# Optimization experiments

Measured on AMD Instinct MI355X. Metric: run time of the kernel, lower is better.

## Reference

```python
import jax, jax.numpy as jnp
import numpy as np

B, C, H, W = 32, 64, 96, 96
RED = 8


def setup_inputs() -> dict:
    key = jax.random.key(0)
    k0, k1, k2 = jax.random.split(key, 3)
    x = jax.random.normal(k0, (B, C, H, W), dtype=jnp.float32)
    # 1x1 conv weights (squeezed to linear): conv1 C->C//RED, conv2 C//RED->C
    w1 = jax.random.normal(k1, (C // RED, C), dtype=jnp.float32) * (1.0 / np.sqrt(C))
    b1 = jnp.zeros((C // RED,), dtype=jnp.float32)
    w2 = jax.random.normal(k2, (C, C // RED), dtype=jnp.float32) * (1.0 / np.sqrt(C // RED))
    b2 = jnp.zeros((C,), dtype=jnp.float32)
    return {"x": x, "w1": w1, "b1": b1, "w2": w2, "b2": b2}


def reference(x, w1, b1, w2, b2):
    Bx, Cx, Hx, Wx = x.shape
    M = Hx * Wx
    # --- covariance pooling: x @ I_hat @ x^T == centered outer product / M ---
    xr = x.reshape(Bx, Cx, M)
    xc = xr - xr.mean(axis=-1, keepdims=True)
    cov = jnp.einsum('bcm,bdm->bcd', xc, xc) / M  # (B, C, C)
    # --- Newton-Schulz matrix sqrt, iteration = 5 ---
    I3 = 3.0 * jnp.eye(Cx, dtype=x.dtype)  # broadcast over batch
    normA = jnp.trace(cov, axis1=1, axis2=2)  # (1/3 * cov * 3I).sum == trace
    A = cov / normA[:, None, None]
    ZY = 0.5 * (I3 - A)
    Y = A @ ZY
    Z = ZY
    for _ in range(3):  # range(1, iteration-1) with iteration=5
        ZY = (0.5 * (I3 - Z)) @ Y
        Y = Y @ ZY
        Z = ZY @ Z
    ZY = 0.5 * (Y @ (I3 - Z @ Y))
    cov_sqrt = ZY * jnp.sqrt(normA)[:, None, None]  # (B, C, C)
    # --- channel gating ---
    s = cov_sqrt.mean(axis=1)  # mean over dim=1 -> (B, C)
    h = jax.nn.relu(s @ w1.T + b1)
    gate = jax.nn.sigmoid(h @ w2.T + b2)  # (B, C)
    return x * gate[:, :, None, None]
```

## Files before the change

### kernel.cpp

```cpp
#include <hip/hip_runtime.h>
#include <math.h>


#define BB 32
#define CC 64
#define MM 9216
#define NCHUNKS 16

typedef __attribute__((ext_vector_type(8))) short bf16x8;
typedef __attribute__((ext_vector_type(4))) float f32x4;

__device__ __forceinline__ short f2bf(float f) {
  unsigned u = __builtin_bit_cast(unsigned, f);
  return (short)(unsigned short)((u + 0x8000u) >> 16);
}
__device__ __forceinline__ float bf2f(short h) {
  unsigned u = ((unsigned)(unsigned short)h) << 16;
  return __builtin_bit_cast(float, u);
}
__device__ __forceinline__ void wt_store(float* p, float v) {
  __hip_atomic_store(p, v, __ATOMIC_RELAXED, __HIP_MEMORY_SCOPE_AGENT);
}

template <int NSTEP>
__device__ __forceinline__ void gram_body(const float* __restrict__ xb, int mwave,
                                          int quad, int col,
                                          f32x4 acc[4][4], float csum[4]) {
  const float* base[4];
#pragma unroll
  for (int rb = 0; rb < 4; rb++)
    base[rb] = xb + (size_t)(rb * 16 + col) * MM + mwave + quad * 8;

  float4 cur[4][2];
#pragma unroll
  for (int rb = 0; rb < 4; rb++) {
    cur[rb][0] = *(const float4*)(base[rb]);
    cur[rb][1] = *(const float4*)(base[rb] + 4);
  }
#pragma unroll
  for (int s = 0; s < NSTEP; s++) {
    float4 nxt[4][2];
    if (s + 1 < NSTEP) {
#pragma unroll
      for (int rb = 0; rb < 4; rb++) {
        const float* p = base[rb] + (s + 1) * 32;
        nxt[rb][0] = *(const float4*)(p);
        nxt[rb][1] = *(const float4*)(p + 4);
      }
    }
    bf16x8 frag[4];
#pragma unroll
    for (int rb = 0; rb < 4; rb++) {
      float v0 = cur[rb][0].x, v1 = cur[rb][0].y, v2 = cur[rb][0].z, v3 = cur[rb][0].w;
      float v4 = cur[rb][1].x, v5 = cur[rb][1].y, v6 = cur[rb][1].z, v7 = cur[rb][1].w;
      csum[rb] += ((v0 + v1) + (v2 + v3)) + ((v4 + v5) + (v6 + v7));
      bf16x8 f;
      f[0] = f2bf(v0); f[1] = f2bf(v1); f[2] = f2bf(v2); f[3] = f2bf(v3);
      f[4] = f2bf(v4); f[5] = f2bf(v5); f[6] = f2bf(v6); f[7] = f2bf(v7);
      frag[rb] = f;
    }
#pragma unroll
    for (int i = 0; i < 4; i++)
#pragma unroll
      for (int j = 0; j < 4; j++)
        acc[i][j] = __builtin_amdgcn_mfma_f32_16x16x32_bf16(frag[i], frag[j],
                                                            acc[i][j], 0, 0, 0);
    if (s + 1 < NSTEP) {
#pragma unroll
      for (int rb = 0; rb < 4; rb++) {
        cur[rb][0] = nxt[rb][0];
        cur[rb][1] = nxt[rb][1];
      }
    }
  }
}

__device__ __forceinline__ void mm64(short* __restrict__ D, const short* __restrict__ A,
                                     const short* __restrict__ Bm, int tid) {
  int w = tid >> 6, lane = tid & 63, quad = lane >> 4, col = lane & 15;
  f32x4 acc[4];
#pragma unroll
  for (int j = 0; j < 4; j++) acc[j] = (f32x4){0.f, 0.f, 0.f, 0.f};
#pragma unroll
  for (int ks = 0; ks < 2; ks++) {
    int k0 = ks * 32 + quad * 8;
    bf16x8 fa = *(const bf16x8*)(A + (w * 16 + col) * 64 + k0);
#pragma unroll
    for (int j = 0; j < 4; j++) {
      bf16x8 fb = *(const bf16x8*)(Bm + (j * 16 + col) * 64 + k0);
      acc[j] = __builtin_amdgcn_mfma_f32_16x16x32_bf16(fa, fb, acc[j], 0, 0, 0);
    }
  }
#pragma unroll
  for (int j = 0; j < 4; j++)
#pragma unroll
    for (int r = 0; r < 4; r++)
      D[(w * 16 + quad * 4 + r) * 64 + j * 16 + col] = f2bf(acc[j][r]);
}

__device__ __forceinline__ void mmcolsum(const short* __restrict__ A,
                                         const short* __restrict__ Bm,
                                         float* scol, int tid) {
  int w = tid >> 6, lane = tid & 63, quad = lane >> 4, col = lane & 15;
  f32x4 acc[4];
#pragma unroll
  for (int j = 0; j < 4; j++) acc[j] = (f32x4){0.f, 0.f, 0.f, 0.f};
#pragma unroll
  for (int ks = 0; ks < 2; ks++) {
    int k0 = ks * 32 + quad * 8;
    bf16x8 fa = *(const bf16x8*)(A + (w * 16 + col) * 64 + k0);
#pragma unroll
    for (int j = 0; j < 4; j++) {
      bf16x8 fb = *(const bf16x8*)(Bm + (j * 16 + col) * 64 + k0);
      acc[j] = __builtin_amdgcn_mfma_f32_16x16x32_bf16(fa, fb, acc[j], 0, 0, 0);
    }
  }
#pragma unroll
  for (int j = 0; j < 4; j++) {
    float t = (acc[j][0] + acc[j][1]) + (acc[j][2] + acc[j][3]);
    atomicAdd(&scol[j * 16 + col], t);
  }
}

__device__ __forceinline__ void ns_tail(unsigned char* smem, int b, int tid,
                                        const float* __restrict__ pg,
                                        const float* __restrict__ ps,
                                        const float* __restrict__ w1,
                                        const float* __restrict__ pb1,
                                        const float* __restrict__ w2,
                                        const float* __restrict__ pb2,
                                        float* __restrict__ gatews) {
  short* nb0 = (short*)smem;
  short* nb1 = nb0 + 4096;
  short* nb2 = nb0 + 8192;
  short* nb3 = nb0 + 12288;
  short* nb4 = nb0 + 16384;
  float* gsum = (float*)(smem + 40960);
  float* mu = (float*)(smem + 57344);
  float* scol = (float*)(smem + 57600);
  float* hbuf = (float*)(smem + 57856);
  float* pnorm = (float*)(smem + 57888);

  {
    const float4* pgb4 = (const float4*)(pg + (size_t)b * NCHUNKS * 4096);
    float4* gsum4 = (float4*)gsum;
#pragma unroll
    for (int e = 0; e < 4; e++) {
      int i4 = tid + 256 * e;
      float4 s = {0.f, 0.f, 0.f, 0.f};
#pragma unroll
      for (int c = 0; c < NCHUNKS; c++) {
        float4 v = pgb4[c * 1024 + i4];
        s.x += v.x; s.y += v.y; s.z += v.z; s.w += v.w;
      }
      gsum4[i4] = s;
    }
    if (tid < 64) {
      const float* psb = ps + (size_t)b * NCHUNKS * 256;
      float s = 0.f;
#pragma unroll
      for (int c = 0; c < NCHUNKS; c++)
#pragma unroll
        for (int sub = 0; sub < 4; sub++) s += psb[c * 256 + sub * 64 + tid];
      mu[tid] = s * (1.0f / MM);
    }
  }
  __syncthreads();

  if (tid < 64) {
    float d = gsum[tid * 65] * (1.0f / MM) - mu[tid] * mu[tid];
#pragma unroll
    for (int off = 32; off >= 1; off >>= 1) d += __shfl_down(d, off);
    if (tid == 0) *pnorm = d;
  }
  __syncthreads();
  float normA = *pnorm;
  float rn = 1.0f / normA;
#pragma unroll
  for (int e = 0; e < 16; e++) {
    int idx = tid + 256 * e;
    int r = idx >> 6, c = idx & 63;
    float cv = gsum[idx] * (1.0f / MM) - mu[r] * mu[c];
    float a = cv * rn;
    nb0[idx] = f2bf(a);
    nb1[idx] = f2bf((r == c ? 1.5f : 0.0f) - 0.5f * a);
  }
  __syncthreads();
  mm64(nb2, nb0, nb1, tid);
  __syncthreads();
  short *pY = nb2, *pZ = nb1, *s0 = nb3, *s1 = nb4, *s2 = nb0;
  for (int it = 0; it < 3; ++it) {
#pragma unroll
    for (int e = 0; e < 16; e++) {
      int idx = tid + 256 * e;
      int r = idx >> 6, c = idx & 63;
      float z = bf2f(pZ[idx]);
      s0[idx] = f2bf((r == c ? 1.5f : 0.0f) - 0.5f * z);
    }
    __syncthreads();
    mm64(s1, s0, pY, tid);
    __syncthreads();
    mm64(s2, pY, s1, tid);
    mm64(s0, s1, pZ, tid);
    __syncthreads();
    short* oY = pY; short* oZ = pZ; short* oW = s1;
    pY = s2; pZ = s0; s0 = oY; s1 = oZ; s2 = oW;
  }
  mm64(s0, pZ, pY, tid);
  __syncthreads();
#pragma unroll
  for (int e = 0; e < 16; e++) {
    int idx = tid + 256 * e;
    int r = idx >> 6, c = idx & 63;
    float p = bf2f(s0[idx]);
    s0[idx] = f2bf((r == c ? 3.0f : 0.0f) - p);
  }
  if (tid < 64) scol[tid] = 0.0f;
  __syncthreads();
  mmcolsum(pY, s0, scol, tid);
  __syncthreads();
  if (tid < 8) {
    float sc = 0.5f * sqrtf(normA) * (1.0f / 64.0f);
    float acc2 = pb1[tid];
    for (int c = 0; c < 64; c++) acc2 += scol[c] * sc * w1[tid * 64 + c];
    hbuf[tid] = fmaxf(acc2, 0.0f);
  }
  __syncthreads();
  if (tid < 64) {
    float acc2 = pb2[tid];
#pragma unroll
    for (int j = 0; j < 8; j++) acc2 += hbuf[j] * w2[tid * 8 + j];
    gatews[b * 64 + tid] = 1.0f / (1.0f + __expf(-acc2));
  }
}

__global__ __launch_bounds__(256, 2) void gramns_k(
    const float* __restrict__ x, float* __restrict__ pg, float* __restrict__ ps,
    int* __restrict__ ctr, const float* __restrict__ w1,
    const float* __restrict__ pb1, const float* __restrict__ w2,
    const float* __restrict__ pb2, float* __restrict__ gatews) {
  __shared__ __align__(16) unsigned char smem[65536];
  float(*red)[4096] = reinterpret_cast<float(*)[4096]>(smem);

  int b = blockIdx.x / NCHUNKS;
  int chunk = blockIdx.x % NCHUNKS;
  int tid = threadIdx.x;
  int w = tid >> 6, lane = tid & 63;
  int quad = lane >> 4, col = lane & 15;
  const float* xb = x + (size_t)b * CC * MM;

  f32x4 acc[4][4];
#pragma unroll
  for (int i = 0; i < 4; i++)
#pragma unroll
    for (int j = 0; j < 4; j++) acc[i][j] = (f32x4){0.f, 0.f, 0.f, 0.f};
  float csum[4] = {0.f, 0.f, 0.f, 0.f};

  if (chunk < 8) {
    int mwave = chunk * 640 + w * (5 * 32);
    gram_body<5>(xb, mwave, quad, col, acc, csum);
  } else {
    int mwave = 5120 + (chunk - 8) * 512 + w * (4 * 32);
    gram_body<4>(xb, mwave, quad, col, acc, csum);
  }

#pragma unroll
  for (int rb = 0; rb < 4; rb++) {
    float c0 = csum[rb];
    c0 += __shfl_xor(c0, 16);
    c0 += __shfl_xor(c0, 32);
    if (lane < 16)
      wt_store(ps + (size_t)blockIdx.x * 256 + w * 64 + rb * 16 + lane, c0);
  }

#pragma unroll
  for (int i = 0; i < 4; i++)
#pragma unroll
    for (int j = 0; j < 4; j++)
#pragma unroll
      for (int r = 0; r < 4; r++)
        red[w][(i * 16 + quad * 4 + r) * 64 + j * 16 + col] = acc[i][j][r];
  __syncthreads();
  float* covb = pg + (size_t)blockIdx.x * 4096;
#pragma unroll
  for (int e = 0; e < 16; e++) {
    int idx = tid + 256 * e;
    float v = (red[0][idx] + red[1][idx]) + (red[2][idx] + red[3][idx]);
    wt_store(covb + idx, v);
  }

  __syncthreads();
  volatile int* pold = (int*)smem;
  if (tid == 0)
    *pold = __hip_atomic_fetch_add(ctr + b, 1, __ATOMIC_RELAXED,
                                   __HIP_MEMORY_SCOPE_AGENT);
  __syncthreads();
  if (*pold != NCHUNKS - 1) return;

  __builtin_amdgcn_fence(__ATOMIC_ACQUIRE, "agent");
  ns_tail(smem, b, tid, pg, ps, w1, pb1, w2, pb2, gatews);
}

__global__ __launch_bounds__(256) void gate_mul(const float* __restrict__ x,
                                                const float* __restrict__ gatews,
                                                float* __restrict__ out) {
  int bc = blockIdx.x;
  float g = gatews[bc];
  const float4* xp = (const float4*)(x + (size_t)bc * MM);
  float4* op = (float4*)(out + (size_t)bc * MM);
  int t = threadIdx.x;
#pragma unroll
  for (int it = 0; it < 9; ++it) {
    float4 v = xp[t + it * 256];
    v.x *= g; v.y *= g; v.z *= g; v.w *= g;
    op[t + it * 256] = v;
  }
}

__global__ __launch_bounds__(256, 2) void gram_k_leg(const float* __restrict__ x,
                                                     float* __restrict__ pg,
                                                     float* __restrict__ ps) {
  int b = blockIdx.x / NCHUNKS;
  int chunk = blockIdx.x % NCHUNKS;
  int tid = threadIdx.x;
  int w = tid >> 6, lane = tid & 63;
  int quad = lane >> 4, col = lane & 15;
  const float* xb = x + (size_t)b * CC * MM;

  f32x4 acc[4][4];
#pragma unroll
  for (int i = 0; i < 4; i++)
#pragma unroll
    for (int j = 0; j < 4; j++) acc[i][j] = (f32x4){0.f, 0.f, 0.f, 0.f};
  float csum[4] = {0.f, 0.f, 0.f, 0.f};
  if (chunk < 8) {
    int mwave = chunk * 640 + w * (5 * 32);
    gram_body<5>(xb, mwave, quad, col, acc, csum);
  } else {
    int mwave = 5120 + (chunk - 8) * 512 + w * (4 * 32);
    gram_body<4>(xb, mwave, quad, col, acc, csum);
  }
#pragma unroll
  for (int rb = 0; rb < 4; rb++) {
    float c0 = csum[rb];
    c0 += __shfl_xor(c0, 16);
    c0 += __shfl_xor(c0, 32);
    if (lane < 16)
      ps[(size_t)blockIdx.x * 256 + w * 64 + rb * 16 + lane] = c0;
  }
  __shared__ float red[4][4096];
#pragma unroll
  for (int i = 0; i < 4; i++)
#pragma unroll
    for (int j = 0; j < 4; j++)
#pragma unroll
      for (int r = 0; r < 4; r++)
        red[w][(i * 16 + quad * 4 + r) * 64 + j * 16 + col] = acc[i][j][r];
  __syncthreads();
  float* covb = pg + (size_t)blockIdx.x * 4096;
#pragma unroll
  for (int e = 0; e < 16; e++) {
    int idx = tid + 256 * e;
    covb[idx] = (red[0][idx] + red[1][idx]) + (red[2][idx] + red[3][idx]);
  }
}

__global__ __launch_bounds__(256) void ns_k_leg(const float* __restrict__ pg,
                                                const float* __restrict__ ps,
                                                const float* __restrict__ w1,
                                                const float* __restrict__ pb1,
                                                const float* __restrict__ w2,
                                                const float* __restrict__ pb2,
                                                float* __restrict__ gatews) {
  __shared__ __align__(16) unsigned char smem[60416];
  ns_tail(smem, blockIdx.x, threadIdx.x, pg, ps, w1, pb1, w2, pb2, gatews);
}

extern "C" void kernel_launch(void* const* d_in, const int* in_sizes, int n_in,
                              void* d_out, int out_size, void* d_ws, size_t ws_size,
                              hipStream_t stream) {
  const float* x = (const float*)d_in[0];
  const float* w1 = (const float*)d_in[1];
  const float* b1 = (const float*)d_in[2];
  const float* w2 = (const float*)d_in[3];
  const float* b2 = (const float*)d_in[4];
  float* out = (float*)d_out;
  float* ws = (float*)d_ws;

  const size_t NPG = (size_t)BB * NCHUNKS * 4096;
  const size_t NPS = (size_t)BB * NCHUNKS * 256;
  float* pg = ws;
  float* psum = ws + NPG;
  float* gatews = psum + NPS;
  int* ctr = (int*)(gatews + BB * CC);
  const size_t needP = (NPG + NPS + BB * CC + BB) * sizeof(float);

  if (ws_size >= needP) {
    hipMemsetAsync(ctr, 0, BB * sizeof(int), stream);
    gramns_k<<<BB * NCHUNKS, 256, 0, stream>>>(x, pg, psum, ctr, w1, b1, w2,
                                               b2, gatews);
    gate_mul<<<BB * CC, 256, 0, stream>>>(x, gatews, out);
  } else {
    gram_k_leg<<<BB * NCHUNKS, 256, 0, stream>>>(x, pg, psum);
    ns_k_leg<<<BB, 256, 0, stream>>>(pg, psum, w1, b1, w2, b2, gatews);
    gate_mul<<<BB * CC, 256, 0, stream>>>(x, gatews, out);
  }
}
```

Measured before the change: 174.7 us.

## Fuse gate multiply into gram kernel with per-batch spin-wait on gate flag

```diff
diff --git a/kernel.cpp b/kernel.cpp
--- a/kernel.cpp
+++ b/kernel.cpp
@@ -20,6 +20,15 @@
 }
 __device__ __forceinline__ void wt_store(float* p, float v) {
   __hip_atomic_store(p, v, __ATOMIC_RELAXED, __HIP_MEMORY_SCOPE_AGENT);
+}
+__device__ __forceinline__ float ag_load(const float* p) {
+  return __hip_atomic_load(p, __ATOMIC_RELAXED, __HIP_MEMORY_SCOPE_AGENT);
+}
+__device__ __forceinline__ float2 ag_load2(const float* p) {
+  unsigned long long u = __hip_atomic_load((const unsigned long long*)p,
+                                           __ATOMIC_RELAXED,
+                                           __HIP_MEMORY_SCOPE_AGENT);
+  return __builtin_bit_cast(float2, u);
 }
 
 template <int NSTEP>
@@ -121,6 +130,8 @@
     atomicAdd(&scol[j * 16 + col], t);
   }
 }
+
+#define GATE_SH_OFF 57920
 
 __device__ __forceinline__ void ns_tail(unsigned char* smem, int b, int tid,
                                         const float* __restrict__ pg,
@@ -140,20 +151,21 @@
   float* scol = (float*)(smem + 57600);
   float* hbuf = (float*)(smem + 57856);
   float* pnorm = (float*)(smem + 57888);
+  float* gate_sh = (float*)(smem + GATE_SH_OFF);
 
   {
-    const float4* pgb4 = (const float4*)(pg + (size_t)b * NCHUNKS * 4096);
-    float4* gsum4 = (float4*)gsum;
-#pragma unroll
-    for (int e = 0; e < 4; e++) {
-      int i4 = tid + 256 * e;
-      float4 s = {0.f, 0.f, 0.f, 0.f};
+    const float* pgb = pg + (size_t)b * NCHUNKS * 4096;
+#pragma unroll
+    for (int e = 0; e < 8; e++) {
+      int i2 = tid + 256 * e;
+      float sx = 0.f, sy = 0.f;
 #pragma unroll
       for (int c = 0; c < NCHUNKS; c++) {
-        float4 v = pgb4[c * 1024 + i4];
-        s.x += v.x; s.y += v.y; s.z += v.z; s.w += v.w;
+        float2 v = ag_load2(pgb + c * 4096 + 2 * i2);
+        sx += v.x; sy += v.y;
       }
-      gsum4[i4] = s;
+      gsum[2 * i2] = sx;
+      gsum[2 * i2 + 1] = sy;
     }
     if (tid < 64) {
       const float* psb = ps + (size_t)b * NCHUNKS * 256;
@@ -161,7 +173,8 @@
 #pragma unroll
       for (int c = 0; c < NCHUNKS; c++)
 #pragma unroll
-        for (int sub = 0; sub < 4; sub++) s += psb[c * 256 + sub * 64 + tid];
+        for (int sub = 0; sub < 4; sub++)
+          s += ag_load(psb + c * 256 + sub * 64 + tid);
       mu[tid] = s * (1.0f / MM);
     }
   }
@@ -230,15 +243,39 @@
     float acc2 = pb2[tid];
 #pragma unroll
     for (int j = 0; j < 8; j++) acc2 += hbuf[j] * w2[tid * 8 + j];
-    gatews[b * 64 + tid] = 1.0f / (1.0f + __expf(-acc2));
-  }
-}
-
-__global__ __launch_bounds__(256, 2) void gramns_k(
+    float g = 1.0f / (1.0f + __expf(-acc2));
+    gate_sh[tid] = g;
+    wt_store(gatews + b * 64 + tid, g);
+  }
+}
+
+template <int W4>
+__device__ __forceinline__ void gate_phase(const float* __restrict__ x,
+                                           float* __restrict__ out, int b,
+                                           int m0, int tid,
+                                           const float* gate_sh) {
+  const float4* xp = (const float4*)x;
+  float4* op = (float4*)out;
+  size_t base = (size_t)b * CC * (MM / 4) + (m0 >> 2);
+#pragma unroll
+  for (int k = 0; k < (64 * W4) / 256; k++) {
+    int i = tid + 256 * k;
+    int c = i / W4;
+    int off = i - c * W4;
+    float g = gate_sh[c];
+    size_t idx = base + (size_t)c * (MM / 4) + off;
+    float4 v = xp[idx];
+    v.x *= g; v.y *= g; v.z *= g; v.w *= g;
+    op[idx] = v;
+  }
+}
+
+__global__ __launch_bounds__(256, 2) void fused_k(
     const float* __restrict__ x, float* __restrict__ pg, float* __restrict__ ps,
-    int* __restrict__ ctr, const float* __restrict__ w1,
+    int* __restrict__ ctr, int* __restrict__ flag, const float* __restrict__ w1,
     const float* __restrict__ pb1, const float* __restrict__ w2,
-    const float* __restrict__ pb2, float* __restrict__ gatews) {
+    const float* __restrict__ pb2, float* __restrict__ gatews,
+    float* __restrict__ out) {
   __shared__ __align__(16) unsigned char smem[65536];
   float(*red)[4096] = reinterpret_cast<float(*)[4096]>(smem);
 
@@ -256,12 +293,13 @@
     for (int j = 0; j < 4; j++) acc[i][j] = (f32x4){0.f, 0.f, 0.f, 0.f};
   float csum[4] = {0.f, 0.f, 0.f, 0.f};
 
+  int m0;
   if (chunk < 8) {
-    int mwave = chunk * 640 + w * (5 * 32);
-    gram_body<5>(xb, mwave, quad, col, acc, csum);
+    m0 = chunk * 640;
+    gram_body<5>(xb, m0 + w * 160, quad, col, acc, csum);
   } else {
-    int mwave = 5120 + (chunk - 8) * 512 + w * (4 * 32);
-    gram_body<4>(xb, mwave, quad, col, acc, csum);
+    m0 = 5120 + (chunk - 8) * 512;
+    gram_body<4>(xb, m0 + w * 128, quad, col, acc, csum);
   }
 
 #pragma unroll
@@ -295,26 +333,31 @@
     *pold = __hip_atomic_fetch_add(ctr + b, 1, __ATOMIC_RELAXED,
                                    __HIP_MEMORY_SCOPE_AGENT);
   __syncthreads();
-  if (*pold != NCHUNKS - 1) return;
-
-  __builtin_amdgcn_fence(__ATOMIC_ACQUIRE, "agent");
-  ns_tail(smem, b, tid, pg, ps, w1, pb1, w2, pb2, gatews);
-}
-
-__global__ __launch_bounds__(256) void gate_mul(const float* __restrict__ x,
-                                                const float* __restrict__ gatews,
-                                                float* __restrict__ out) {
-  int bc = blockIdx.x;
-  float g = gatews[bc];
-  const float4* xp = (const float4*)(x + (size_t)bc * MM);
-  float4* op = (float4*)(out + (size_t)bc * MM);
-  int t = threadIdx.x;
-#pragma unroll
-  for (int it = 0; it < 9; ++it) {
-    float4 v = xp[t + it * 256];
-    v.x *= g; v.y *= g; v.z *= g; v.w *= g;
-    op[t + it * 256] = v;
-  }
+  int oldv = *pold;
+  __syncthreads();
+
+  float* gate_sh = (float*)(smem + GATE_SH_OFF);
+  if (oldv == NCHUNKS - 1) {
+    ns_tail(smem, b, tid, pg, ps, w1, pb1, w2, pb2, gatews);
+    __syncthreads();
+    if (tid == 0)
+      __hip_atomic_store(flag + b, 1, __ATOMIC_RELAXED,
+                         __HIP_MEMORY_SCOPE_AGENT);
+  } else {
+    if (tid == 0) {
+      while (__hip_atomic_load(flag + b, __ATOMIC_RELAXED,
+                               __HIP_MEMORY_SCOPE_AGENT) == 0)
+        __builtin_amdgcn_s_sleep(8);
+    }
+    __syncthreads();
+    if (tid < 64) gate_sh[tid] = ag_load(gatews + b * 64 + tid);
+    __syncthreads();
+  }
+
+  if (chunk < 8)
+    gate_phase<160>(x, out, b, m0, tid, gate_sh);
+  else
+    gate_phase<128>(x, out, b, m0, tid, gate_sh);
 }
 
 __global__ __launch_bounds__(256, 2) void gram_k_leg(const float* __restrict__ x,
@@ -334,11 +377,9 @@
     for (int j = 0; j < 4; j++) acc[i][j] = (f32x4){0.f, 0.f, 0.f, 0.f};
   float csum[4] = {0.f, 0.f, 0.f, 0.f};
   if (chunk < 8) {
-    int mwave = chunk * 640 + w * (5 * 32);
-    gram_body<5>(xb, mwave, quad, col, acc, csum);
+    gram_body<5>(xb, chunk * 640 + w * 160, quad, col, acc, csum);
   } else {
-    int mwave = 5120 + (chunk - 8) * 512 + w * (4 * 32);
-    gram_body<4>(xb, mwave, quad, col, acc, csum);
+    gram_body<4>(xb, 5120 + (chunk - 8) * 512 + w * 128, quad, col, acc, csum);
   }
 #pragma unroll
   for (int rb = 0; rb < 4; rb++) {
@@ -374,6 +415,22 @@
                                                 float* __restrict__ gatews) {
   __shared__ __align__(16) unsigned char smem[60416];
   ns_tail(smem, blockIdx.x, threadIdx.x, pg, ps, w1, pb1, w2, pb2, gatews);
+}
+
+__global__ __launch_bounds__(256) void gate_mul_leg(const float* __restrict__ x,
+                                                    const float* __restrict__ gatews,
+                                                    float* __restrict__ out) {
+  int bc = blockIdx.x;
+  float g = gatews[bc];
+  const float4* xp = (const float4*)(x + (size_t)bc * MM);
+  float4* op = (float4*)(out + (size_t)bc * MM);
+  int t = threadIdx.x;
+#pragma unroll
+  for (int it = 0; it < 9; ++it) {
+    float4 v = xp[t + it * 256];
+    v.x *= g; v.y *= g; v.z *= g; v.w *= g;
+    op[t + it * 256] = v;
+  }
 }
 
 extern "C" void kernel_launch(void* const* d_in, const int* in_sizes, int n_in,
@@ -393,16 +450,16 @@
   float* psum = ws + NPG;
   float* gatews = psum + NPS;
   int* ctr = (int*)(gatews + BB * CC);
-  const size_t needP = (NPG + NPS + BB * CC + BB) * sizeof(float);
+  int* flag = ctr + BB;
+  const size_t needP = (NPG + NPS + BB * CC + 2 * BB) * sizeof(float);
 
   if (ws_size >= needP) {
-    hipMemsetAsync(ctr, 0, BB * sizeof(int), stream);
-    gramns_k<<<BB * NCHUNKS, 256, 0, stream>>>(x, pg, psum, ctr, w1, b1, w2,
-                                               b2, gatews);
-    gate_mul<<<BB * CC, 256, 0, stream>>>(x, gatews, out);
+    hipMemsetAsync(ctr, 0, 2 * BB * sizeof(int), stream);
+    fused_k<<<BB * NCHUNKS, 256, 0, stream>>>(x, pg, psum, ctr, flag, w1, b1,
+                                              w2, b2, gatews, out);
   } else {
     gram_k_leg<<<BB * NCHUNKS, 256, 0, stream>>>(x, pg, psum);
     ns_k_leg<<<BB, 256, 0, stream>>>(pg, psum, w1, b1, w2, b2, gatews);
-    gate_mul<<<BB * CC, 256, 0, stream>>>(x, gatews, out);
-  }
-}
+    gate_mul_leg<<<BB * CC, 256, 0, stream>>>(x, gatews, out);
+  }
+}
```

Measured after the change: 169.3 us. 1.03x faster.
